# Kernel optimization log

Hardware: AMD Instinct MI355X
Metric: run time of the kernel (lower is better)

The kernel has to match this reference:

```python
import jax, jax.numpy as jnp
import numpy as np

D = 128   # node feature dim
C = 2     # classes
N = 50000 # nodes
E = 500000  # edges (before self-loops)
H1 = 2    # conv1 heads
NEG_SLOPE = 0.2
BN_EPS = 1e-5


def setup_inputs() -> dict:
    key = jax.random.key(0)
    ks = jax.random.split(key, 24)
    rn = lambda k, shape, s=0.05: jax.random.normal(k, shape, dtype=jnp.float32) * s
    inp = {
        'x': jax.random.normal(ks[0], (N, D), dtype=jnp.float32),
        'edge_index': jax.random.randint(ks[1], (2, E), 0, N, dtype=jnp.int64),
        # conv1: GATConv(D, D, heads=2, concat=True)
        'W1': rn(ks[2], (D, H1 * D)),
        'att_src1': rn(ks[3], (H1, D)),
        'att_dst1': rn(ks[4], (H1, D)),
        'bias1': jnp.zeros((H1 * D,), jnp.float32),
        # conv2: GATConv(2D, D, heads=1, concat=False)
        'W2': rn(ks[5], (2 * D, D)),
        'att_src2': rn(ks[6], (1, D)),
        'att_dst2': rn(ks[7], (1, D)),
        'bias2': jnp.zeros((D,), jnp.float32),
        # lin1 = MLP([3D, 96]) : Linear -> ReLU -> BatchNorm1d
        'Wl': rn(ks[8], (3 * D, 96)), 'bl': jnp.zeros((96,), jnp.float32),
        'gl': jnp.ones((96,), jnp.float32), 'betal': jnp.zeros((96,), jnp.float32),
        # mlp1 = MLP([96, 96, C]) : two (Linear -> ReLU -> BN) blocks
        'Wa': rn(ks[9], (96, 96)), 'ba': jnp.zeros((96,), jnp.float32),
        'ga': jnp.ones((96,), jnp.float32), 'betaa': jnp.zeros((96,), jnp.float32),
        'Wb': rn(ks[10], (96, C)), 'bb': jnp.zeros((C,), jnp.float32),
        'gb': jnp.ones((C,), jnp.float32), 'betab': jnp.zeros((C,), jnp.float32),
    }
    return inp


def gat_conv(x, src, dst, W, att_src, att_dst, bias, heads, out_dim, concat):
    # PyG GATConv: h = x W -> [N,H,F]; per-edge logit leakyrelu(a_s.h_src + a_d.h_dst);
    # segment softmax over edges grouped by destination; weighted scatter-sum.
    n = x.shape[0]
    h = (x @ W).reshape(n, heads, out_dim)
    a_src = jnp.einsum('nhd,hd->nh', h, att_src)  # [N,H]
    a_dst = jnp.einsum('nhd,hd->nh', h, att_dst)
    alpha = jax.nn.leaky_relu(a_src[src] + a_dst[dst], NEG_SLOPE)  # [Etot,H]
    m = jax.ops.segment_max(alpha, dst, num_segments=n)            # [N,H]
    e = jnp.exp(alpha - m[dst])
    s = jax.ops.segment_sum(e, dst, num_segments=n)
    w = e / (s[dst] + 1e-16)                                       # [Etot,H]
    out = jax.ops.segment_sum(h[src] * w[:, :, None], dst, num_segments=n)  # [N,H,F]
    out = out.reshape(n, heads * out_dim) if concat else out.mean(axis=1)
    return out + bias


def mlp_block(x, W, b, gamma, beta):
    # Linear -> ReLU -> BatchNorm1d (training-mode batch stats, biased var)
    y = jax.nn.relu(x @ W + b)
    mu = y.mean(axis=0)
    var = ((y - mu) ** 2).mean(axis=0)
    return gamma * (y - mu) / jnp.sqrt(var + BN_EPS) + beta


def reference(x, edge_index, W1, att_src1, att_dst1, bias1,
              W2, att_src2, att_dst2, bias2,
              Wl, bl, gl, betal, Wa, ba, ga, betaa, Wb, bb, gb, betab):
    n = x.shape[0]
    # PyG GATConv default add_self_loops=True
    loops = jnp.arange(n, dtype=edge_index.dtype)
    src = jnp.concatenate([edge_index[0], loops])
    dst = jnp.concatenate([edge_index[1], loops])
    x1 = gat_conv(x, src, dst, W1, att_src1, att_dst1, bias1, H1, D, True)    # [N,2D]
    x2 = gat_conv(x1, src, dst, W2, att_src2, att_dst2, bias2, 1, D, False)   # [N,D]
    h = jnp.concatenate([x1, x2], axis=1)                                      # [N,3D]
    h = mlp_block(h, Wl, bl, gl, betal)     # lin1
    h = mlp_block(h, Wa, ba, ga, betaa)     # mlp1 layer 1
    h = mlp_block(h, Wb, bb, gb, betab)     # mlp1 layer 2
    return h
```

## Files before the change

kernel.cpp:

```cpp
#include <hip/hip_runtime.h>
#include <hip/hip_bf16.h>
#include <cstdint>
#include <cstddef>

#define NNODES 50000
#define NEDGES 500000
#define ETOT   (NEDGES + NNODES)
#define MAXDEG 96

typedef __attribute__((ext_vector_type(8))) short short8;
typedef __attribute__((ext_vector_type(8))) unsigned short ushort8v;
typedef __attribute__((ext_vector_type(4))) float floatx4;
typedef __attribute__((ext_vector_type(4))) unsigned short ushort4v;

__device__ __forceinline__ unsigned short f2bf(float f) {
    union { __hip_bfloat16 h; unsigned short u; } cv;
    cv.h = __float2bfloat16(f);
    return cv.u;
}
__device__ __forceinline__ float bf2f(unsigned short u) {
    union { unsigned int i; float f; } cv;
    cv.i = ((unsigned int)u) << 16;
    return cv.f;
}

#define GBM 128
#define GBN 64
#define GBK 32

__global__ __launch_bounds__(256, 4) void gemm_mfma(
    const unsigned short* __restrict__ A, int lda,
    const unsigned short* __restrict__ Bt,
    float* __restrict__ C,
    unsigned short* __restrict__ Cb, int ldc,
    const float* __restrict__ bias,
    float* __restrict__ colsum, float* __restrict__ colsq,
    const float* __restrict__ att_s, const float* __restrict__ att_d,
    float* __restrict__ as_out, float* __restrict__ ad_out, int Hheads,
    int M, int N, int K, int do_relu)
{
    __shared__ __attribute__((aligned(16))) unsigned short Alds[GBM * GBK];
    __shared__ __attribute__((aligned(16))) unsigned short Blds[GBN * GBK];
    __shared__ float scol[GBN], sqcol[GBN];

    int tid = threadIdx.x;
    int wave = tid >> 6, lane = tid & 63;
    int row0 = blockIdx.y * GBM;
    int col0 = blockIdx.x * GBN;
    int m = lane & 15, q = lane >> 4;

    floatx4 acc[2][4] = {};

    for (int k0 = 0; k0 < K; k0 += GBK) {
        #pragma unroll
        for (int i = 0; i < 2; ++i) {
            int c = tid + i * 256;
            int r = c >> 2, off = (c & 3) * 8;
            int gr = row0 + r;
            short8 v = {};
            if (gr < M) v = *(const short8*)(A + (size_t)gr * lda + k0 + off);
            *(short8*)(Alds + r * GBK + off) = v;
        }
        {
            int r = tid >> 2, off = (tid & 3) * 8;
            short8 v = *(const short8*)(Bt + (size_t)(col0 + r) * K + k0 + off);
            *(short8*)(Blds + r * GBK + off) = v;
        }
        __syncthreads();

        short8 a0 = *(const short8*)(Alds + (wave * 32 + m) * GBK + q * 8);
        short8 a1 = *(const short8*)(Alds + (wave * 32 + 16 + m) * GBK + q * 8);
        #pragma unroll
        for (int ct = 0; ct < 4; ++ct) {
            short8 b = *(const short8*)(Blds + (ct * 16 + m) * GBK + q * 8);
            acc[0][ct] = __builtin_amdgcn_mfma_f32_16x16x32_bf16(a0, b, acc[0][ct], 0, 0, 0);
            acc[1][ct] = __builtin_amdgcn_mfma_f32_16x16x32_bf16(a1, b, acc[1][ct], 0, 0, 0);
        }
        __syncthreads();
    }

    float ps[4] = {}, pq[4] = {};
    #pragma unroll
    for (int rt = 0; rt < 2; ++rt) {
        #pragma unroll
        for (int r = 0; r < 4; ++r) {
            int gr = row0 + wave * 32 + rt * 16 + q * 4 + r;
            float ds = 0.f, dd = 0.f;
            #pragma unroll
            for (int ct = 0; ct < 4; ++ct) {
                int gc = col0 + ct * 16 + m;
                float v = acc[rt][ct][r];
                if (gc < N) {
                    float vb = v;
                    if (bias != nullptr) vb += bias[gc];
                    if (do_relu) vb = fmaxf(vb, 0.f);
                    if (att_s != nullptr) { ds += vb * att_s[gc]; dd += vb * att_d[gc]; }
                    if (gr < M) {
                        if (C  != nullptr) C[(size_t)gr * ldc + gc] = vb;
                        if (Cb != nullptr) Cb[(size_t)gr * ldc + gc] = f2bf(vb);
                        ps[ct] += vb; pq[ct] += vb * vb;
                    }
                }
            }
            if (att_s != nullptr) {
                #pragma unroll
                for (int off = 1; off < 16; off <<= 1) {
                    ds += __shfl_xor(ds, off);
                    dd += __shfl_xor(dd, off);
                }
                if (m == 0 && gr < M) {
                    int head = col0 >> 7;
                    atomicAdd(&as_out[gr * Hheads + head], ds);
                    atomicAdd(&ad_out[gr * Hheads + head], dd);
                }
            }
        }
    }
    if (colsum != nullptr) {
        if (tid < GBN) { scol[tid] = 0.f; sqcol[tid] = 0.f; }
        __syncthreads();
        #pragma unroll
        for (int ct = 0; ct < 4; ++ct) {
            atomicAdd(&scol[ct * 16 + m], ps[ct]);
            atomicAdd(&sqcol[ct * 16 + m], pq[ct]);
        }
        __syncthreads();
        if (tid < GBN) {
            int gc = col0 + tid;
            if (gc < N) {
                atomicAdd(&colsum[gc], scol[tid]);
                atomicAdd(&colsq[gc], sqcol[tid]);
            }
        }
    }
}

__global__ __launch_bounds__(256) void fold_att(
    const float* __restrict__ W1, const float* __restrict__ as1v, const float* __restrict__ ad1v,
    const float* __restrict__ W2, const float* __restrict__ as2v, const float* __restrict__ ad2v,
    float* __restrict__ U1, float* __restrict__ U2)
{
    int g = threadIdx.x >> 5, l = threadIdx.x & 31;
    int task = blockIdx.x * 8 + g;
    float ss = 0.f, sd = 0.f;
    if (task < 256) {
        int d = task & 127, h = task >> 7;
        const float4 wv = *(const float4*)(W1 + d * 256 + h * 128 + l * 4);
        const float4 av = *(const float4*)(as1v + h * 128 + l * 4);
        const float4 bv = *(const float4*)(ad1v + h * 128 + l * 4);
        ss = wv.x * av.x + wv.y * av.y + wv.z * av.z + wv.w * av.w;
        sd = wv.x * bv.x + wv.y * bv.y + wv.z * bv.z + wv.w * bv.w;
    } else {
        int k = task - 256;
        const float4 wv = *(const float4*)(W2 + (size_t)k * 128 + l * 4);
        const float4 av = *(const float4*)(as2v + l * 4);
        const float4 bv = *(const float4*)(ad2v + l * 4);
        ss = wv.x * av.x + wv.y * av.y + wv.z * av.z + wv.w * av.w;
        sd = wv.x * bv.x + wv.y * bv.y + wv.z * bv.z + wv.w * bv.w;
    }
    #pragma unroll
    for (int off = 1; off < 32; off <<= 1) { ss += __shfl_xor(ss, off); sd += __shfl_xor(sd, off); }
    if (l == 0) {
        if (task < 256) {
            int d = task & 127, h = task >> 7;
            U1[h * 128 + d] = ss;
            U1[256 + h * 128 + d] = sd;
        } else {
            int k = task - 256;
            U2[k] = ss;
            U2[256 + k] = sd;
        }
    }
}

__global__ __launch_bounds__(256) void cast_x_att(
    const float* __restrict__ x, const float* __restrict__ U1,
    unsigned short* __restrict__ xb, float* __restrict__ as1, float* __restrict__ ad1)
{
    __shared__ float Us[512];
    int tid = threadIdx.x;
    Us[tid] = U1[tid];
    Us[tid + 256] = U1[tid + 256];
    __syncthreads();
    int g = tid >> 5, l = tid & 31;
    int n = blockIdx.x * 8 + g;
    if (n >= NNODES) return;
    const float4 v = *(const float4*)(x + (size_t)n * 128 + l * 4);
    ushort4v o;
    o.x = f2bf(v.x); o.y = f2bf(v.y); o.z = f2bf(v.z); o.w = f2bf(v.w);
    *(ushort4v*)(xb + (size_t)n * 128 + l * 4) = o;
    const float4 us0 = *(const float4*)(Us + l * 4);
    const float4 us1 = *(const float4*)(Us + 128 + l * 4);
    const float4 ud0 = *(const float4*)(Us + 256 + l * 4);
    const float4 ud1 = *(const float4*)(Us + 384 + l * 4);
    float s0 = v.x * us0.x + v.y * us0.y + v.z * us0.z + v.w * us0.w;
    float s1 = v.x * us1.x + v.y * us1.y + v.z * us1.z + v.w * us1.w;
    float d0 = v.x * ud0.x + v.y * ud0.y + v.z * ud0.z + v.w * ud0.w;
    float d1 = v.x * ud1.x + v.y * ud1.y + v.z * ud1.z + v.w * ud1.w;
    #pragma unroll
    for (int off = 1; off < 32; off <<= 1) {
        s0 += __shfl_xor(s0, off); s1 += __shfl_xor(s1, off);
        d0 += __shfl_xor(d0, off); d1 += __shfl_xor(d1, off);
    }
    if (l == 0) {
        as1[n * 2] = s0; as1[n * 2 + 1] = s1;
        ad1[n * 2] = d0; ad1[n * 2 + 1] = d1;
    }
}

__global__ void cast_weights(const float* __restrict__ W1, const float* __restrict__ W2,
                             const float* __restrict__ Wl,
                             unsigned short* __restrict__ W1t, unsigned short* __restrict__ W2t,
                             unsigned short* __restrict__ Wlt) {
    int i = blockIdx.x * 256 + threadIdx.x;
    if (i < 32768) {
        int n = i >> 7, k = i & 127;
        W1t[i] = f2bf(W1[k * 256 + n]);
    } else if (i < 65536) {
        int j = i - 32768;
        int n = j >> 8, k = j & 255;
        W2t[j] = f2bf(W2[k * 128 + n]);
    } else if (i < 114688) {
        int j = i - 65536;
        int n = j / 384, k = j % 384;
        Wlt[j] = (n < 96) ? f2bf(Wl[(size_t)k * 96 + n]) : (unsigned short)0;
    }
}

__global__ void bnfold_a(const float* __restrict__ csum, const float* __restrict__ csq,
                         const float* __restrict__ gamma, const float* __restrict__ beta,
                         const float* __restrict__ Wa, const float* __restrict__ ba,
                         unsigned short* __restrict__ Wat2, float* __restrict__ ba_f) {
    __shared__ float scl[96], shf[96];
    int tid = threadIdx.x;
    if (tid < 96) {
        float mu  = csum[tid] / (float)NNODES;
        float var = csq[tid] / (float)NNODES - mu * mu;
        if (var < 0.f) var = 0.f;
        float sc = gamma[tid] * rsqrtf(var + 1e-5f);
        scl[tid] = sc; shf[tid] = beta[tid] - mu * sc;
    }
    __syncthreads();
    for (int idx = tid; idx < 128 * 96; idx += 256) {
        int n = idx / 96, k = idx % 96;
        Wat2[idx] = (n < 96) ? f2bf(scl[k] * Wa[k * 96 + n]) : (unsigned short)0;
    }
    if (tid < 96) {
        float s = ba[tid];
        for (int k = 0; k < 96; ++k) s += shf[k] * Wa[k * 96 + tid];
        ba_f[tid] = s;
    }
}

__global__ void bnfold_b(const float* __restrict__ csum, const float* __restrict__ csq,
                         const float* __restrict__ gamma, const float* __restrict__ beta,
                         const float* __restrict__ Wb, const float* __restrict__ bb,
                         unsigned short* __restrict__ Wbt, float* __restrict__ bb_f) {
    __shared__ float scl[96], shf[96];
    int tid = threadIdx.x;
    if (tid < 96) {
        float mu  = csum[tid] / (float)NNODES;
        float var = csq[tid] / (float)NNODES - mu * mu;
        if (var < 0.f) var = 0.f;
        float sc = gamma[tid] * rsqrtf(var + 1e-5f);
        scl[tid] = sc; shf[tid] = beta[tid] - mu * sc;
    }
    __syncthreads();
    for (int idx = tid; idx < 64 * 96; idx += 256) {
        int n = idx / 96, k = idx % 96;
        Wbt[idx] = (n < 2) ? f2bf(scl[k] * Wb[k * 2 + n]) : (unsigned short)0;
    }
    if (tid < 2) {
        float s = bb[tid];
        for (int k = 0; k < 96; ++k) s += shf[k] * Wb[k * 2 + tid];
        bb_f[tid] = s;
    }
}

__global__ void bn_fin_apply(const float* __restrict__ csum, const float* __restrict__ csq,
                             const float* __restrict__ gamma, const float* __restrict__ beta,
                             float* __restrict__ y, int total) {
    int i = blockIdx.x * blockDim.x + threadIdx.x;
    if (i >= total) return;
    int j = i & 1;
    float mu  = csum[j] / (float)NNODES;
    float var = csq[j] / (float)NNODES - mu * mu;
    if (var < 0.f) var = 0.f;
    float sc = gamma[j] * rsqrtf(var + 1e-5f);
    float sh = beta[j] - mu * sc;
    y[i] = y[i] * sc + sh;
}

__device__ __forceinline__ void edge_src_dst(const int* ei, int e, int& src, int& dst) {
    if (e < NEDGES) { src = ei[e]; dst = ei[NEDGES + e]; }
    else { src = e - NEDGES; dst = src; }
}

__global__ __launch_bounds__(256) void csr_count(const int* __restrict__ ei, int* __restrict__ cnt) {
    int e = blockIdx.x * blockDim.x + threadIdx.x;
    if (e >= ETOT) return;
    int src, dst; edge_src_dst(ei, e, src, dst); (void)src;
    atomicAdd(&cnt[dst], 1);
}

#define SCAN_CH 1024
#define SCAN_NB ((NNODES + SCAN_CH - 1) / SCAN_CH)

__global__ __launch_bounds__(256) void scan1(const int* __restrict__ cnt, int* __restrict__ part) {
    int t = threadIdx.x;
    int base = blockIdx.x * SCAN_CH + t * 4;
    int4 v = {0, 0, 0, 0};
    if (base + 3 < NNODES) v = *(const int4*)(cnt + base);
    else {
        if (base + 0 < NNODES) v.x = cnt[base + 0];
        if (base + 1 < NNODES) v.y = cnt[base + 1];
        if (base + 2 < NNODES) v.z = cnt[base + 2];
        if (base + 3 < NNODES) v.w = cnt[base + 3];
    }
    int s = v.x + v.y + v.z + v.w;
    __shared__ int sm[256];
    sm[t] = s;
    __syncthreads();
    for (int off = 128; off > 0; off >>= 1) {
        if (t < off) sm[t] += sm[t + off];
        __syncthreads();
    }
    if (t == 0) part[blockIdx.x] = sm[0];
}

__global__ void scan2(int* __restrict__ part, int* __restrict__ rowstart) {
    int lane = threadIdx.x;
    int v = (lane < SCAN_NB) ? part[lane] : 0;
    #pragma unroll
    for (int off = 1; off < 64; off <<= 1) {
        int t = __shfl_up(v, off);
        if (lane >= off) v += t;
    }
    int ex = __shfl_up(v, 1);
    if (lane == 0) ex = 0;
    if (lane < SCAN_NB) part[lane] = ex;
    if (lane == 0) rowstart[NNODES] = ETOT;
}

__global__ __launch_bounds__(256) void scan3(const int* __restrict__ cnt, const int* __restrict__ part,
                                             int* __restrict__ rowstart, int* __restrict__ cursor) {
    int t = threadIdx.x;
    int base = blockIdx.x * SCAN_CH + t * 4;
    int4 v = {0, 0, 0, 0};
    if (base + 3 < NNODES) v = *(const int4*)(cnt + base);
    else {
        if (base + 0 < NNODES) v.x = cnt[base + 0];
        if (base + 1 < NNODES) v.y = cnt[base + 1];
        if (base + 2 < NNODES) v.z = cnt[base + 2];
        if (base + 3 < NNODES) v.w = cnt[base + 3];
    }
    int s = v.x + v.y + v.z + v.w;
    __shared__ int sm[2][256];
    sm[0][t] = s;
    __syncthreads();
    int cur = 0;
    #pragma unroll
    for (int off = 1; off < 256; off <<= 1) {
        int nxt = cur ^ 1;
        int val = sm[cur][t];
        if (t >= off) val += sm[cur][t - off];
        sm[nxt][t] = val;
        __syncthreads();
        cur = nxt;
    }
    int p = sm[cur][t] - s + part[blockIdx.x];
    if (base + 0 < NNODES) { rowstart[base + 0] = p; cursor[base + 0] = p; } p += v.x;
    if (base + 1 < NNODES) { rowstart[base + 1] = p; cursor[base + 1] = p; } p += v.y;
    if (base + 2 < NNODES) { rowstart[base + 2] = p; cursor[base + 2] = p; } p += v.z;
    if (base + 3 < NNODES) { rowstart[base + 3] = p; cursor[base + 3] = p; }
}

__global__ __launch_bounds__(256) void csr_fill(const int* __restrict__ ei,
                                                int* __restrict__ cursor,
                                                int* __restrict__ esrc) {
    int e = blockIdx.x * blockDim.x + threadIdx.x;
    if (e >= ETOT) return;
    int src, dst; edge_src_dst(ei, e, src, dst);
    int pos = atomicAdd(&cursor[dst], 1);
    esrc[pos] = src;
}

__global__ __launch_bounds__(256) void gat_gather_x2(
    const int* __restrict__ rowstart, const int* __restrict__ esrc,
    const unsigned short* __restrict__ xb, const float* __restrict__ a_src,
    const float* __restrict__ a_dst, unsigned short* __restrict__ xaggh)
{
    __shared__ float wl[4][2][MAXDEG];
    __shared__ int   esl[4][MAXDEG];
    int wave = threadIdx.x >> 6;
    int n = (blockIdx.x * blockDim.x + threadIdx.x) >> 6;
    int lane = threadIdx.x & 63;
    if (n >= NNODES) return;
    int beg = rowstart[n], end = rowstart[n + 1];
    int deg = end - beg;
    float ad0 = a_dst[n * 2], ad1 = a_dst[n * 2 + 1];

    float m0 = -1e30f, m1 = -1e30f;
    for (int idx = lane; idx < deg; idx += 64) {
        int s = esrc[beg + idx];
        float l0 = a_src[s * 2] + ad0;     l0 = l0 >= 0.f ? l0 : 0.2f * l0;
        float l1 = a_src[s * 2 + 1] + ad1; l1 = l1 >= 0.f ? l1 : 0.2f * l1;
        m0 = fmaxf(m0, l0); m1 = fmaxf(m1, l1);
        if (idx < MAXDEG) { wl[wave][0][idx] = l0; wl[wave][1][idx] = l1; esl[wave][idx] = s; }
    }
    #pragma unroll
    for (int off = 1; off < 64; off <<= 1) {
        m0 = fmaxf(m0, __shfl_xor(m0, off));
        m1 = fmaxf(m1, __shfl_xor(m1, off));
    }
    float s0 = 0.f, s1 = 0.f;
    for (int idx = lane; idx < deg; idx += 64) {
        float l0, l1;
        if (idx < MAXDEG) { l0 = wl[wave][0][idx]; l1 = wl[wave][1][idx]; }
        else {
            int s = esrc[beg + idx];
            l0 = a_src[s * 2] + ad0;     l0 = l0 >= 0.f ? l0 : 0.2f * l0;
            l1 = a_src[s * 2 + 1] + ad1; l1 = l1 >= 0.f ? l1 : 0.2f * l1;
        }
        float e0 = __expf(l0 - m0), e1 = __expf(l1 - m1);
        s0 += e0; s1 += e1;
        if (idx < MAXDEG) { wl[wave][0][idx] = e0; wl[wave][1][idx] = e1; }
    }
    #pragma unroll
    for (int off = 1; off < 64; off <<= 1) {
        s0 += __shfl_xor(s0, off);
        s1 += __shfl_xor(s1, off);
    }
    float inv0 = 1.f / (s0 + 1e-16f), inv1 = 1.f / (s1 + 1e-16f);

    int g  = lane >> 4;
    int sl = lane & 15;

    float a0[8] = {}, a1[8] = {}, b0[8] = {}, b1[8] = {};
    for (int idx = g; idx < deg; idx += 8) {
        int sA; float wA0, wA1;
        if (idx < MAXDEG) {
            sA = esl[wave][idx];
            wA0 = wl[wave][0][idx] * inv0; wA1 = wl[wave][1][idx] * inv1;
        } else {
            sA = esrc[beg + idx];
            float l0 = a_src[sA * 2] + ad0;     l0 = l0 >= 0.f ? l0 : 0.2f * l0;
            float l1 = a_src[sA * 2 + 1] + ad1; l1 = l1 >= 0.f ? l1 : 0.2f * l1;
            wA0 = __expf(l0 - m0) * inv0; wA1 = __expf(l1 - m1) * inv1;
        }
        const ushort8v hvA = *(const ushort8v*)(xb + (size_t)sA * 128 + sl * 8);
        int i2 = idx + 4;
        if (i2 < deg) {
            int sB; float wB0, wB1;
            if (i2 < MAXDEG) {
                sB = esl[wave][i2];
                wB0 = wl[wave][0][i2] * inv0; wB1 = wl[wave][1][i2] * inv1;
            } else {
                sB = esrc[beg + i2];
                float l0 = a_src[sB * 2] + ad0;     l0 = l0 >= 0.f ? l0 : 0.2f * l0;
                float l1 = a_src[sB * 2 + 1] + ad1; l1 = l1 >= 0.f ? l1 : 0.2f * l1;
                wB0 = __expf(l0 - m0) * inv0; wB1 = __expf(l1 - m1) * inv1;
            }
            const ushort8v hvB = *(const ushort8v*)(xb + (size_t)sB * 128 + sl * 8);
            #pragma unroll
            for (int j = 0; j < 8; ++j) {
                float f = bf2f(hvB[j]);
                b0[j] += wB0 * f; b1[j] += wB1 * f;
            }
        }
        #pragma unroll
        for (int j = 0; j < 8; ++j) {
            float f = bf2f(hvA[j]);
            a0[j] += wA0 * f; a1[j] += wA1 * f;
        }
    }
    #pragma unroll
    for (int j = 0; j < 8; ++j) { a0[j] += b0[j]; a1[j] += b1[j]; }
    #pragma unroll
    for (int j = 0; j < 8; ++j) {
        a0[j] += __shfl_xor(a0[j], 16); a0[j] += __shfl_xor(a0[j], 32);
        a1[j] += __shfl_xor(a1[j], 16); a1[j] += __shfl_xor(a1[j], 32);
    }
    if (g == 0) {
        ushort8v o0, o1;
        #pragma unroll
        for (int j = 0; j < 8; ++j) { o0[j] = f2bf(a0[j]); o1[j] = f2bf(a1[j]); }
        *(ushort8v*)(xaggh + (size_t)n * 256 + sl * 8) = o0;
        *(ushort8v*)(xaggh + (size_t)n * 256 + 128 + sl * 8) = o1;
    }
}

__global__ __launch_bounds__(256) void gat_gather_h1(
    const int* __restrict__ rowstart, const int* __restrict__ esrc,
    const unsigned short* __restrict__ hb, const float* __restrict__ a_src,
    const float* __restrict__ a_dst, const float* __restrict__ bias,
    unsigned short* __restrict__ xcat)
{
    __shared__ float wl[4][MAXDEG];
    __shared__ int   esl[4][MAXDEG];
    int wave = threadIdx.x >> 6;
    int n = (blockIdx.x * blockDim.x + threadIdx.x) >> 6;
    int lane = threadIdx.x & 63;
    if (n >= NNODES) return;
    int beg = rowstart[n], end = rowstart[n + 1];
    int deg = end - beg;
    float ad0 = a_dst[n];

    float m0 = -1e30f;
    for (int idx = lane; idx < deg; idx += 64) {
        int s = esrc[beg + idx];
        float l0 = a_src[s] + ad0; l0 = l0 >= 0.f ? l0 : 0.2f * l0;
        m0 = fmaxf(m0, l0);
        if (idx < MAXDEG) { wl[wave][idx] = l0; esl[wave][idx] = s; }
    }
    #pragma unroll
    for (int off = 1; off < 64; off <<= 1) m0 = fmaxf(m0, __shfl_xor(m0, off));
    float s0 = 0.f;
    for (int idx = lane; idx < deg; idx += 64) {
        float l0;
        if (idx < MAXDEG) l0 = wl[wave][idx];
        else {
            int s = esrc[beg + idx];
            l0 = a_src[s] + ad0; l0 = l0 >= 0.f ? l0 : 0.2f * l0;
        }
        float e0 = __expf(l0 - m0);
        s0 += e0;
        if (idx < MAXDEG) wl[wave][idx] = e0;
    }
    #pragma unroll
    for (int off = 1; off < 64; off <<= 1) s0 += __shfl_xor(s0, off);
    float inv0 = 1.f / (s0 + 1e-16f);

    int g  = lane >> 4;
    int sl = lane & 15;

    float acc[8] = {}, acc2[8] = {};
    for (int idx = g; idx < deg; idx += 8) {
        int sA; float wA;
        if (idx < MAXDEG) { sA = esl[wave][idx]; wA = wl[wave][idx] * inv0; }
        else {
            sA = esrc[beg + idx];
            float l = a_src[sA] + ad0; l = l >= 0.f ? l : 0.2f * l;
            wA = __expf(l - m0) * inv0;
        }
        const ushort8v hvA = *(const ushort8v*)(hb + (size_t)sA * 128 + sl * 8);
        int i2 = idx + 4;
        if (i2 < deg) {
            int sB; float wB;
            if (i2 < MAXDEG) { sB = esl[wave][i2]; wB = wl[wave][i2] * inv0; }
            else {
                sB = esrc[beg + i2];
                float l = a_src[sB] + ad0; l = l >= 0.f ? l : 0.2f * l;
                wB = __expf(l - m0) * inv0;
            }
            const ushort8v hvB = *(const ushort8v*)(hb + (size_t)sB * 128 + sl * 8);
            #pragma unroll
            for (int j = 0; j < 8; ++j) acc2[j] += wB * bf2f(hvB[j]);
        }
        #pragma unroll
        for (int j = 0; j < 8; ++j) acc[j] += wA * bf2f(hvA[j]);
    }
    #pragma unroll
    for (int j = 0; j < 8; ++j) acc[j] += acc2[j];
    #pragma unroll
    for (int j = 0; j < 8; ++j) acc[j] += __shfl_xor(acc[j], 16);
    #pragma unroll
    for (int j = 0; j < 8; ++j) acc[j] += __shfl_xor(acc[j], 32);
    if (g == 0) {
        ushort8v o;
        #pragma unroll
        for (int j = 0; j < 8; ++j) o[j] = f2bf(acc[j] + bias[sl * 8 + j]);
        *(ushort8v*)(xcat + (size_t)n * 384 + 256 + sl * 8) = o;
    }
}

extern "C" void kernel_launch(void* const* d_in, const int* in_sizes, int n_in,
                              void* d_out, int out_size, void* d_ws, size_t ws_size,
                              hipStream_t stream) {
    const float* x        = (const float*)d_in[0];
    const int*   ei       = (const int*)d_in[1];
    const float* W1       = (const float*)d_in[2];
    const float* att_src1 = (const float*)d_in[3];
    const float* att_dst1 = (const float*)d_in[4];
    const float* bias1    = (const float*)d_in[5];
    const float* W2       = (const float*)d_in[6];
    const float* att_src2 = (const float*)d_in[7];
    const float* att_dst2 = (const float*)d_in[8];
    const float* bias2    = (const float*)d_in[9];
    const float* Wl       = (const float*)d_in[10];
    const float* bl       = (const float*)d_in[11];
    const float* gl       = (const float*)d_in[12];
    const float* betal    = (const float*)d_in[13];
    const float* Wa       = (const float*)d_in[14];
    const float* ba       = (const float*)d_in[15];
    const float* ga       = (const float*)d_in[16];
    const float* betaa    = (const float*)d_in[17];
    const float* Wb       = (const float*)d_in[18];
    const float* bb       = (const float*)d_in[19];
    const float* gb       = (const float*)d_in[20];
    const float* betab    = (const float*)d_in[21];
    float* out = (float*)d_out;
    char* ws = (char*)d_ws;

    const int N = NNODES;

    const size_t offY2b  = 0;
    const size_t offXcat = 19200000;
    const size_t offXb   = 57600000;
    const size_t offY1b  = 70400000;
    const size_t offXagg = 80000000;
    const size_t offW1t  = 105600000;
    const size_t offW2t  = 105665536;
    const size_t offWlt  = 105731072;
    const size_t offWat2 = 105829376;
    const size_t offWbt  = 105853952;
    const size_t offBaf  = 105866240;
    const size_t offBbf  = 105866640;
    const size_t offU1   = 105867264;
    const size_t offU2   = 105869312;
    const size_t offRow  = 106000000;
    const size_t offCur  = 106200128;
    const size_t offEsrc = 106400832;
    const size_t offPart = 108700000;
    const size_t offAs1  = 108800000;
    const size_t offAd1  = 109200000;
    const size_t offAs2  = 109600000;
    const size_t offAd2  = 109800000;
    const size_t offSt   = 110000000;

    unsigned short* y2b   = (unsigned short*)(ws + offY2b);
    unsigned short* xcat  = (unsigned short*)(ws + offXcat);
    unsigned short* xb    = (unsigned short*)(ws + offXb);
    unsigned short* hb2   = (unsigned short*)(ws + offXb);
    unsigned short* y1b   = (unsigned short*)(ws + offY1b);
    unsigned short* xaggh = (unsigned short*)(ws + offXagg);
    unsigned short* W1t   = (unsigned short*)(ws + offW1t);
    unsigned short* W2t   = (unsigned short*)(ws + offW2t);
    unsigned short* Wlt   = (unsigned short*)(ws + offWlt);
    unsigned short* Wat2  = (unsigned short*)(ws + offWat2);
    unsigned short* Wbt   = (unsigned short*)(ws + offWbt);
    float* ba_f = (float*)(ws + offBaf);
    float* bb_f = (float*)(ws + offBbf);
    float* U1   = (float*)(ws + offU1);
    float* U2   = (float*)(ws + offU2);
    int* rowst  = (int*)(ws + offRow);
    int* cursor = (int*)(ws + offCur);
    int* esrc   = (int*)(ws + offEsrc);
    int* part   = (int*)(ws + offPart);
    float* as1  = (float*)(ws + offAs1);
    float* ad1  = (float*)(ws + offAd1);
    float* as2  = (float*)(ws + offAs2);
    float* ad2  = (float*)(ws + offAd2);

    float* csum_l = (float*)(ws + offSt + 0);
    float* csq_l  = (float*)(ws + offSt + 512);
    float* csum_a = (float*)(ws + offSt + 2048);
    float* csq_a  = (float*)(ws + offSt + 2560);
    float* csum_b = (float*)(ws + offSt + 4096);
    float* csq_b  = (float*)(ws + offSt + 4608);

    hipMemsetAsync(ws + offRow, 0, (NNODES + 1) * sizeof(int), stream);
    hipMemsetAsync(ws + offAs1, 0, (offSt + 6144) - offAs1, stream);

    dim3 blk(256);
    int edgeBlocks  = (ETOT + 255) / 256;
    int waveBlocksN = (N + 3) / 4;
    dim3 gemmRows((N + GBM - 1) / GBM);

    fold_att<<<64, blk, 0, stream>>>(W1, att_src1, att_dst1, W2, att_src2, att_dst2, U1, U2);
    cast_x_att<<<(N + 7) / 8, blk, 0, stream>>>(x, U1, xb, as1, ad1);
    cast_weights<<<(114688 + 255) / 256, blk, 0, stream>>>(W1, W2, Wl, W1t, W2t, Wlt);

    csr_count<<<edgeBlocks, blk, 0, stream>>>(ei, rowst);
    scan1<<<SCAN_NB, blk, 0, stream>>>(rowst, part);
    scan2<<<1, 64, 0, stream>>>(part, rowst);
    scan3<<<SCAN_NB, blk, 0, stream>>>(rowst, part, rowst, cursor);
    csr_fill<<<edgeBlocks, blk, 0, stream>>>(ei, cursor, esrc);

    gat_gather_x2<<<waveBlocksN, blk, 0, stream>>>(rowst, esrc, xb, as1, ad1, xaggh);
    gemm_mfma<<<dim3(2, gemmRows.x), blk, 0, stream>>>(
        xaggh, 256, W1t, nullptr, xcat, 384, bias1, nullptr, nullptr,
        U2, U2 + 256, as2, ad2, 1, N, 128, 128, 0);
    gemm_mfma<<<dim3(2, gemmRows.x), blk, 0, stream>>>(
        xaggh + 128, 256, W1t + 128 * 128, nullptr, xcat + 128, 384, bias1 + 128,
        nullptr, nullptr, U2 + 128, U2 + 384, as2, ad2, 1, N, 128, 128, 0);

    gemm_mfma<<<dim3(2, gemmRows.x), blk, 0, stream>>>(
        xcat, 384, W2t, nullptr, hb2, 128, nullptr, nullptr, nullptr,
        nullptr, nullptr, nullptr, nullptr, 0, N, 128, 256, 0);
    gat_gather_h1<<<waveBlocksN, blk, 0, stream>>>(rowst, esrc, hb2, as2, ad2, bias2, xcat);

    gemm_mfma<<<dim3(2, gemmRows.x), blk, 0, stream>>>(
        xcat, 384, Wlt, nullptr, y1b, 96, bl, csum_l, csq_l,
        nullptr, nullptr, nullptr, nullptr, 0, N, 96, 384, 1);
    bnfold_a<<<1, 256, 0, stream>>>(csum_l, csq_l, gl, betal, Wa, ba, Wat2, ba_f);

    gemm_mfma<<<dim3(2, gemmRows.x), blk, 0, stream>>>(
        y1b, 96, Wat2, nullptr, y2b, 96, ba_f, csum_a, csq_a,
        nullptr, nullptr, nullptr, nullptr, 0, N, 96, 96, 1);
    bnfold_b<<<1, 256, 0, stream>>>(csum_a, csq_a, ga, betaa, Wb, bb, Wbt, bb_f);

    gemm_mfma<<<dim3(1, gemmRows.x), blk, 0, stream>>>(
        y2b, 96, Wbt, out, nullptr, 2, bb_f, csum_b, csq_b,
        nullptr, nullptr, nullptr, nullptr, 0, N, 2, 96, 1);

    bn_fin_apply<<<(N * 2 + 255) / 256, blk, 0, stream>>>(csum_b, csq_b, gb, betab, out, N * 2);
}
```

Before: 410.9 us.

## Map each node to a 16-lane group in GAT gather kernels

Both GAT gather kernels now assign one 16-lane group per destination node instead of a full 64-lane wave, processing 16 nodes per block. For degree up to 16 the logits, softmax and weights stay in registers and are broadcast with width-16 shuffles, which removes shared-memory staging and the cross-group accumulator reductions. The aim is to stop most lanes sitting idle at the average degree of about 11 and to increase node-level parallelism per wave. High-degree nodes take a slower serial fallback that recomputes logits three times.

```diff
diff --git a/kernel.cpp b/kernel.cpp
--- a/kernel.cpp
+++ b/kernel.cpp
@@ -6,7 +6,6 @@
 #define NNODES 50000
 #define NEDGES 500000
 #define ETOT   (NEDGES + NNODES)
-#define MAXDEG 96
 
 typedef __attribute__((ext_vector_type(8))) short short8;
 typedef __attribute__((ext_vector_type(8))) unsigned short ushort8v;
@@ -390,104 +389,111 @@
     const unsigned short* __restrict__ xb, const float* __restrict__ a_src,
     const float* __restrict__ a_dst, unsigned short* __restrict__ xaggh)
 {
-    __shared__ float wl[4][2][MAXDEG];
-    __shared__ int   esl[4][MAXDEG];
-    int wave = threadIdx.x >> 6;
-    int n = (blockIdx.x * blockDim.x + threadIdx.x) >> 6;
-    int lane = threadIdx.x & 63;
+    int tid = threadIdx.x;
+    int t = tid & 15;
+    int n = blockIdx.x * 16 + (tid >> 4);
     if (n >= NNODES) return;
-    int beg = rowstart[n], end = rowstart[n + 1];
-    int deg = end - beg;
-    float ad0 = a_dst[n * 2], ad1 = a_dst[n * 2 + 1];
-
-    float m0 = -1e30f, m1 = -1e30f;
-    for (int idx = lane; idx < deg; idx += 64) {
-        int s = esrc[beg + idx];
-        float l0 = a_src[s * 2] + ad0;     l0 = l0 >= 0.f ? l0 : 0.2f * l0;
-        float l1 = a_src[s * 2 + 1] + ad1; l1 = l1 >= 0.f ? l1 : 0.2f * l1;
-        m0 = fmaxf(m0, l0); m1 = fmaxf(m1, l1);
-        if (idx < MAXDEG) { wl[wave][0][idx] = l0; wl[wave][1][idx] = l1; esl[wave][idx] = s; }
-    }
-    #pragma unroll
-    for (int off = 1; off < 64; off <<= 1) {
-        m0 = fmaxf(m0, __shfl_xor(m0, off));
-        m1 = fmaxf(m1, __shfl_xor(m1, off));
-    }
-    float s0 = 0.f, s1 = 0.f;
-    for (int idx = lane; idx < deg; idx += 64) {
-        float l0, l1;
-        if (idx < MAXDEG) { l0 = wl[wave][0][idx]; l1 = wl[wave][1][idx]; }
-        else {
-            int s = esrc[beg + idx];
-            l0 = a_src[s * 2] + ad0;     l0 = l0 >= 0.f ? l0 : 0.2f * l0;
-            l1 = a_src[s * 2 + 1] + ad1; l1 = l1 >= 0.f ? l1 : 0.2f * l1;
-        }
-        float e0 = __expf(l0 - m0), e1 = __expf(l1 - m1);
-        s0 += e0; s1 += e1;
-        if (idx < MAXDEG) { wl[wave][0][idx] = e0; wl[wave][1][idx] = e1; }
-    }
-    #pragma unroll
-    for (int off = 1; off < 64; off <<= 1) {
-        s0 += __shfl_xor(s0, off);
-        s1 += __shfl_xor(s1, off);
-    }
-    float inv0 = 1.f / (s0 + 1e-16f), inv1 = 1.f / (s1 + 1e-16f);
-
-    int g  = lane >> 4;
-    int sl = lane & 15;
-
-    float a0[8] = {}, a1[8] = {}, b0[8] = {}, b1[8] = {};
-    for (int idx = g; idx < deg; idx += 8) {
-        int sA; float wA0, wA1;
-        if (idx < MAXDEG) {
-            sA = esl[wave][idx];
-            wA0 = wl[wave][0][idx] * inv0; wA1 = wl[wave][1][idx] * inv1;
-        } else {
-            sA = esrc[beg + idx];
-            float l0 = a_src[sA * 2] + ad0;     l0 = l0 >= 0.f ? l0 : 0.2f * l0;
-            float l1 = a_src[sA * 2 + 1] + ad1; l1 = l1 >= 0.f ? l1 : 0.2f * l1;
-            wA0 = __expf(l0 - m0) * inv0; wA1 = __expf(l1 - m1) * inv1;
-        }
-        const ushort8v hvA = *(const ushort8v*)(xb + (size_t)sA * 128 + sl * 8);
-        int i2 = idx + 4;
-        if (i2 < deg) {
-            int sB; float wB0, wB1;
-            if (i2 < MAXDEG) {
-                sB = esl[wave][i2];
-                wB0 = wl[wave][0][i2] * inv0; wB1 = wl[wave][1][i2] * inv1;
-            } else {
-                sB = esrc[beg + i2];
-                float l0 = a_src[sB * 2] + ad0;     l0 = l0 >= 0.f ? l0 : 0.2f * l0;
-                float l1 = a_src[sB * 2 + 1] + ad1; l1 = l1 >= 0.f ? l1 : 0.2f * l1;
-                wB0 = __expf(l0 - m0) * inv0; wB1 = __expf(l1 - m1) * inv1;
-            }
-            const ushort8v hvB = *(const ushort8v*)(xb + (size_t)sB * 128 + sl * 8);
+    int beg = rowstart[n], deg = rowstart[n + 1] - beg;
+    const float2 adv = *(const float2*)(a_dst + n * 2);
+    float acc0[8] = {}, acc1[8] = {};
+
+    if (deg <= 16) {
+        int s = 0; float l0 = -1e30f, l1 = -1e30f;
+        if (t < deg) {
+            s = esrc[beg + t];
+            const float2 asv = *(const float2*)(a_src + s * 2);
+            l0 = asv.x + adv.x; l0 = l0 >= 0.f ? l0 : 0.2f * l0;
+            l1 = asv.y + adv.y; l1 = l1 >= 0.f ? l1 : 0.2f * l1;
+        }
+        float m0 = l0, m1 = l1;
+        #pragma unroll
+        for (int off = 1; off < 16; off <<= 1) {
+            m0 = fmaxf(m0, __shfl_xor(m0, off, 16));
+            m1 = fmaxf(m1, __shfl_xor(m1, off, 16));
+        }
+        float e0 = (t < deg) ? __expf(l0 - m0) : 0.f;
+        float e1 = (t < deg) ? __expf(l1 - m1) : 0.f;
+        float s0 = e0, s1 = e1;
+        #pragma unroll
+        for (int off = 1; off < 16; off <<= 1) {
+            s0 += __shfl_xor(s0, off, 16);
+            s1 += __shfl_xor(s1, off, 16);
+        }
+        float w0 = e0 / (s0 + 1e-16f);
+        float w1 = e1 / (s1 + 1e-16f);
+
+        int e = 0;
+        for (; e + 1 < deg; e += 2) {
+            int   sA  = __shfl(s,  e, 16),     sB  = __shfl(s,  e + 1, 16);
+            float wA0 = __shfl(w0, e, 16),     wB0 = __shfl(w0, e + 1, 16);
+            float wA1 = __shfl(w1, e, 16),     wB1 = __shfl(w1, e + 1, 16);
+            const ushort8v hvA = *(const ushort8v*)(xb + (size_t)sA * 128 + t * 8);
+            const ushort8v hvB = *(const ushort8v*)(xb + (size_t)sB * 128 + t * 8);
             #pragma unroll
             for (int j = 0; j < 8; ++j) {
-                float f = bf2f(hvB[j]);
-                b0[j] += wB0 * f; b1[j] += wB1 * f;
+                float fA = bf2f(hvA[j]), fB = bf2f(hvB[j]);
+                acc0[j] += wA0 * fA + wB0 * fB;
+                acc1[j] += wA1 * fA + wB1 * fB;
             }
         }
-        #pragma unroll
-        for (int j = 0; j < 8; ++j) {
-            float f = bf2f(hvA[j]);
-            a0[j] += wA0 * f; a1[j] += wA1 * f;
-        }
-    }
+        if (e < deg) {
+            int   sA  = __shfl(s,  e, 16);
+            float wA0 = __shfl(w0, e, 16), wA1 = __shfl(w1, e, 16);
+            const ushort8v hvA = *(const ushort8v*)(xb + (size_t)sA * 128 + t * 8);
+            #pragma unroll
+            for (int j = 0; j < 8; ++j) {
+                float fA = bf2f(hvA[j]);
+                acc0[j] += wA0 * fA; acc1[j] += wA1 * fA;
+            }
+        }
+    } else {
+        float m0 = -1e30f, m1 = -1e30f;
+        for (int idx = t; idx < deg; idx += 16) {
+            int s = esrc[beg + idx];
+            const float2 asv = *(const float2*)(a_src + s * 2);
+            float l0 = asv.x + adv.x; l0 = l0 >= 0.f ? l0 : 0.2f * l0;
+            float l1 = asv.y + adv.y; l1 = l1 >= 0.f ? l1 : 0.2f * l1;
+            m0 = fmaxf(m0, l0); m1 = fmaxf(m1, l1);
+        }
+        #pragma unroll
+        for (int off = 1; off < 16; off <<= 1) {
+            m0 = fmaxf(m0, __shfl_xor(m0, off, 16));
+            m1 = fmaxf(m1, __shfl_xor(m1, off, 16));
+        }
+        float s0 = 0.f, s1 = 0.f;
+        for (int idx = t; idx < deg; idx += 16) {
+            int s = esrc[beg + idx];
+            const float2 asv = *(const float2*)(a_src + s * 2);
+            float l0 = asv.x + adv.x; l0 = l0 >= 0.f ? l0 : 0.2f * l0;
+            float l1 = asv.y + adv.y; l1 = l1 >= 0.f ? l1 : 0.2f * l1;
+            s0 += __expf(l0 - m0); s1 += __expf(l1 - m1);
+        }
+        #pragma unroll
+        for (int off = 1; off < 16; off <<= 1) {
+            s0 += __shfl_xor(s0, off, 16);
+            s1 += __shfl_xor(s1, off, 16);
+        }
+        float inv0 = 1.f / (s0 + 1e-16f), inv1 = 1.f / (s1 + 1e-16f);
+        for (int e = 0; e < deg; ++e) {
+            int s = esrc[beg + e];
+            const float2 asv = *(const float2*)(a_src + s * 2);
+            float l0 = asv.x + adv.x; l0 = l0 >= 0.f ? l0 : 0.2f * l0;
+            float l1 = asv.y + adv.y; l1 = l1 >= 0.f ? l1 : 0.2f * l1;
+            float w0 = __expf(l0 - m0) * inv0, w1 = __expf(l1 - m1) * inv1;
+            const ushort8v hv = *(const ushort8v*)(xb + (size_t)s * 128 + t * 8);
+            #pragma unroll
+            for (int j = 0; j < 8; ++j) {
+                float f = bf2f(hv[j]);
+                acc0[j] += w0 * f; acc1[j] += w1 * f;
+            }
+        }
+    }
+
+    ushort8v o0, o1;
     #pragma unroll
-    for (int j = 0; j < 8; ++j) { a0[j] += b0[j]; a1[j] += b1[j]; }
-    #pragma unroll
-    for (int j = 0; j < 8; ++j) {
-        a0[j] += __shfl_xor(a0[j], 16); a0[j] += __shfl_xor(a0[j], 32);
-        a1[j] += __shfl_xor(a1[j], 16); a1[j] += __shfl_xor(a1[j], 32);
-    }
-    if (g == 0) {
-        ushort8v o0, o1;
-        #pragma unroll
-        for (int j = 0; j < 8; ++j) { o0[j] = f2bf(a0[j]); o1[j] = f2bf(a1[j]); }
-        *(ushort8v*)(xaggh + (size_t)n * 256 + sl * 8) = o0;
-        *(ushort8v*)(xaggh + (size_t)n * 256 + 128 + sl * 8) = o1;
-    }
+    for (int j = 0; j < 8; ++j) { o0[j] = f2bf(acc0[j]); o1[j] = f2bf(acc1[j]); }
+    *(ushort8v*)(xaggh + (size_t)n * 256 + t * 8) = o0;
+    *(ushort8v*)(xaggh + (size_t)n * 256 + 128 + t * 8) = o1;
 }
 
 __global__ __launch_bounds__(256) void gat_gather_h1(
@@ -496,82 +502,86 @@
     const float* __restrict__ a_dst, const float* __restrict__ bias,
     unsigned short* __restrict__ xcat)
 {
-    __shared__ float wl[4][MAXDEG];
-    __shared__ int   esl[4][MAXDEG];
-    int wave = threadIdx.x >> 6;
-    int n = (blockIdx.x * blockDim.x + threadIdx.x) >> 6;
-    int lane = threadIdx.x & 63;
+    int tid = threadIdx.x;
+    int t = tid & 15;
+    int n = blockIdx.x * 16 + (tid >> 4);
     if (n >= NNODES) return;
-    int beg = rowstart[n], end = rowstart[n + 1];
-    int deg = end - beg;
+    int beg = rowstart[n], deg = rowstart[n + 1] - beg;
     float ad0 = a_dst[n];
-
-    float m0 = -1e30f;
-    for (int idx = lane; idx < deg; idx += 64) {
-        int s = esrc[beg + idx];
-        float l0 = a_src[s] + ad0; l0 = l0 >= 0.f ? l0 : 0.2f * l0;
-        m0 = fmaxf(m0, l0);
-        if (idx < MAXDEG) { wl[wave][idx] = l0; esl[wave][idx] = s; }
-    }
-    #pragma unroll
-    for (int off = 1; off < 64; off <<= 1) m0 = fmaxf(m0, __shfl_xor(m0, off));
-    float s0 = 0.f;
-    for (int idx = lane; idx < deg; idx += 64) {
-        float l0;
-        if (idx < MAXDEG) l0 = wl[wave][idx];
-        else {
+    float acc[8] = {};
+
+    if (deg <= 16) {
+        int s = 0; float l0 = -1e30f;
+        if (t < deg) {
+            s = esrc[beg + t];
+            l0 = a_src[s] + ad0; l0 = l0 >= 0.f ? l0 : 0.2f * l0;
+        }
+        float m0 = l0;
+        #pragma unroll
+        for (int off = 1; off < 16; off <<= 1)
+            m0 = fmaxf(m0, __shfl_xor(m0, off, 16));
+        float e0 = (t < deg) ? __expf(l0 - m0) : 0.f;
+        float s0 = e0;
+        #pragma unroll
+        for (int off = 1; off < 16; off <<= 1)
+            s0 += __shfl_xor(s0, off, 16);
+        float w0 = e0 / (s0 + 1e-16f);
+
+        int e = 0;
+        for (; e + 1 < deg; e += 2) {
+            int   sA = __shfl(s,  e, 16),  sB = __shfl(s,  e + 1, 16);
+            float wA = __shfl(w0, e, 16),  wB = __shfl(w0, e + 1, 16);
+            const ushort8v hvA = *(const ushort8v*)(hb + (size_t)sA * 128 + t * 8);
+            const ushort8v hvB = *(const ushort8v*)(hb + (size_t)sB * 128 + t * 8);
+            #pragma unroll
+            for (int j = 0; j < 8; ++j)
+                acc[j] += wA * bf2f(hvA[j]) + wB * bf2f(hvB[j]);
+        }
+        if (e < deg) {
+            int   sA = __shfl(s,  e, 16);
+            float wA = __shfl(w0, e, 16);
+            const ushort8v hvA = *(const ushort8v*)(hb + (size_t)sA * 128 + t * 8);
+            #pragma unroll
+            for (int j = 0; j < 8; ++j) acc[j] += wA * bf2f(hvA[j]);
+        }
+    } else {
+        float m0 = -1e30f;
+        for (int idx = t; idx < deg; idx += 16) {
             int s = esrc[beg + idx];
-            l0 = a_src[s] + ad0; l0 = l0 >= 0.f ? l0 : 0.2f * l0;
-        }
-        float e0 = __expf(l0 - m0);
-        s0 += e0;
-        if (idx < MAXDEG) wl[wave][idx] = e0;
-    }
-    #pragma unroll
-    for (int off = 1; off < 64; off <<= 1) s0 += __shfl_xor(s0, off);
-    float inv0 = 1.f / (s0 + 1e-16f);
-
-    int g  = lane >> 4;
-    int sl = lane & 15;
-
-    float acc[8] = {}, acc2[8] = {};
-    for (int idx = g; idx < deg; idx += 8) {
-        int sA; float wA;
-        if (idx < MAXDEG) { sA = esl[wave][idx]; wA = wl[wave][idx] * inv0; }
-        else {
-            sA = esrc[beg + idx];
-            float l = a_src[sA] + ad0; l = l >= 0.f ? l : 0.2f * l;
-            wA = __expf(l - m0) * inv0;
-        }
-        const ushort8v hvA = *(const ushort8v*)(hb + (size_t)sA * 128 + sl * 8);
-        int i2 = idx + 4;
-        if (i2 < deg) {
-            int sB; float wB;
-            if (i2 < MAXDEG) { sB = esl[wave][i2]; wB = wl[wave][i2] * inv0; }
-            else {
-                sB = esrc[beg + i2];
-                float l = a_src[sB] + ad0; l = l >= 0.f ? l : 0.2f * l;
-                wB = __expf(l - m0) * inv0;
-            }
-            const ushort8v hvB = *(const ushort8v*)(hb + (size_t)sB * 128 + sl * 8);
+            float l0 = a_src[s] + ad0; l0 = l0 >= 0.f ? l0 : 0.2f * l0;
+            m0 = fmaxf(m0, l0);
+        }
+        #pragma unroll
+        for (int off = 1; off < 16; off <<= 1)
+            m0 = fmaxf(m0, __shfl_xor(m0, off, 16));
+        float s0 = 0.f;
+        for (int idx = t; idx < deg; idx += 16) {
+            int s = esrc[beg + idx];
+            float l0 = a_src[s] + ad0; l0 = l0 >= 0.f ? l0 : 0.2f * l0;
+            s0 += __expf(l0 - m0);
+        }
+        #pragma unroll
+        for (int off = 1; off < 16; off <<= 1)
+            s0 += __shfl_xor(s0, off, 16);
+        float inv0 = 1.f / (s0 + 1e-16f);
+        for (int e = 0; e < deg; ++e) {
+            int s = esrc[beg + e];
+            float l0 = a_src[s] + ad0; l0 = l0 >= 0.f ? l0 : 0.2f * l0;
+            float w0 = __expf(l0 - m0) * inv0;
+            const ushort8v hv = *(const ushort8v*)(hb + (size_t)s * 128 + t * 8);
             #pragma unroll
-            for (int j = 0; j < 8; ++j) acc2[j] += wB * bf2f(hvB[j]);
-        }
-        #pragma unroll
-        for (int j = 0; j < 8; ++j) acc[j] += wA * bf2f(hvA[j]);
-    }
-    #pragma unroll
-    for (int j = 0; j < 8; ++j) acc[j] += acc2[j];
-    #pragma unroll
-    for (int j = 0; j < 8; ++j) acc[j] += __shfl_xor(acc[j], 16);
-    #pragma unroll
-    for (int j = 0; j < 8; ++j) acc[j] += __shfl_xor(acc[j], 32);
-    if (g == 0) {
-        ushort8v o;
-        #pragma unroll
-        for (int j = 0; j < 8; ++j) o[j] = f2bf(acc[j] + bias[sl * 8 + j]);
-        *(ushort8v*)(xcat + (size_t)n * 384 + 256 + sl * 8) = o;
-    }
+            for (int j = 0; j < 8; ++j) acc[j] += w0 * bf2f(hv[j]);
+        }
+    }
+
+    const float4 b0 = *(const float4*)(bias + t * 8);
+    const float4 b1 = *(const float4*)(bias + t * 8 + 4);
+    ushort8v o;
+    o[0] = f2bf(acc[0] + b0.x); o[1] = f2bf(acc[1] + b0.y);
+    o[2] = f2bf(acc[2] + b0.z); o[3] = f2bf(acc[3] + b0.w);
+    o[4] = f2bf(acc[4] + b1.x); o[5] = f2bf(acc[5] + b1.y);
+    o[6] = f2bf(acc[6] + b1.z); o[7] = f2bf(acc[7] + b1.w);
+    *(ushort8v*)(xcat + (size_t)n * 384 + 256 + t * 8) = o;
 }
 
 extern "C" void kernel_launch(void* const* d_in, const int* in_sizes, int n_in,
@@ -663,8 +673,8 @@
     hipMemsetAsync(ws + offAs1, 0, (offSt + 6144) - offAs1, stream);
 
     dim3 blk(256);
-    int edgeBlocks  = (ETOT + 255) / 256;
-    int waveBlocksN = (N + 3) / 4;
+    int edgeBlocks   = (ETOT + 255) / 256;
+    int nodeBlocks16 = (N + 15) / 16;
     dim3 gemmRows((N + GBM - 1) / GBM);
 
     fold_att<<<64, blk, 0, stream>>>(W1, att_src1, att_dst1, W2, att_src2, att_dst2, U1, U2);
@@ -677,7 +687,7 @@
     scan3<<<SCAN_NB, blk, 0, stream>>>(rowst, part, rowst, cursor);
     csr_fill<<<edgeBlocks, blk, 0, stream>>>(ei, cursor, esrc);
 
-    gat_gather_x2<<<waveBlocksN, blk, 0, stream>>>(rowst, esrc, xb, as1, ad1, xaggh);
+    gat_gather_x2<<<nodeBlocks16, blk, 0, stream>>>(rowst, esrc, xb, as1, ad1, xaggh);
     gemm_mfma<<<dim3(2, gemmRows.x), blk, 0, stream>>>(
         xaggh, 256, W1t, nullptr, xcat, 384, bias1, nullptr, nullptr,
         U2, U2 + 256, as2, ad2, 1, N, 128, 128, 0);
@@ -688,7 +698,7 @@
     gemm_mfma<<<dim3(2, gemmRows.x), blk, 0, stream>>>(
         xcat, 384, W2t, nullptr, hb2, 128, nullptr, nullptr, nullptr,
         nullptr, nullptr, nullptr, nullptr, 0, N, 128, 256, 0);
-    gat_gather_h1<<<waveBlocksN, blk, 0, stream>>>(rowst, esrc, hb2, as2, ad2, bias2, xcat);
+    gat_gather_h1<<<nodeBlocks16, blk, 0, stream>>>(rowst, esrc, hb2, as2, ad2, bias2, xcat);
 
     gemm_mfma<<<dim3(2, gemmRows.x), blk, 0, stream>>>(
         xcat, 384, Wlt, nullptr, y1b, 96, bl, csum_l, csq_l,
```

Result: no change. 412.8 us (+0.5%).
